# Performance work log

Hardware: AMD Instinct MI355X
Metric: run time of the kernel (lower is better)

## Reference

```python
import jax, jax.numpy as jnp
import numpy as np
import math

N_CELLS = 65536
HIDDEN = 128
IN_DIM = 64
MAX_DEG = 6
BOND_P = 0.5


def _build_graph():
    """2D lattice bond percolation -> padded adjacency [n, MAX_DEG] + signs + mask."""
    rng = np.random.default_rng(0)
    side = int(math.ceil(math.sqrt(N_CELLS)))
    adj = [[] for _ in range(N_CELLS)]
    for i in range(N_CELLS):
        col = i % side
        r = i + 1
        if col + 1 < side and r < N_CELLS and rng.random() < BOND_P:
            adj[i].append(r); adj[r].append(i)
        d = i + side
        if d < N_CELLS and rng.random() < BOND_P:
            adj[i].append(d); adj[d].append(i)
    for i in range(N_CELLS):  # ring fix for isolated nodes
        if not adj[i]:
            r = (i + 1) % N_CELLS
            adj[i].append(r); adj[r].append(i)
    sign_map = {}
    for i in range(N_CELLS):
        for j in adj[i]:
            key = (min(i, j), max(i, j))
            if key not in sign_map:
                sign_map[key] = 1.0 if rng.random() > 0.5 else -1.0
    nbr = np.zeros((N_CELLS, MAX_DEG), np.int32)
    sgn = np.ones((N_CELLS, MAX_DEG), np.float32)
    msk = np.zeros((N_CELLS, MAX_DEG), bool)
    for i in range(N_CELLS):
        for k, j in enumerate(adj[i][:MAX_DEG]):
            nbr[i, k] = j
            msk[i, k] = True
            sgn[i, k] = sign_map[(min(i, j), max(i, j))]
    return nbr, sgn, msk


def setup_inputs() -> dict:
    key = jax.random.key(0)
    ks = jax.random.split(key, 8)
    nbr, sgn, msk = _build_graph()
    n = N_CELLS
    cell_amp = jax.random.uniform(ks[0], (n, HIDDEN)) * 0.5 + 0.5
    cell_phase = jax.random.normal(ks[1], (n, HIDDEN)) * 0.5 \
        + (2.0 * jnp.pi * jnp.arange(n, dtype=jnp.float32) / n)[:, None]
    phase_vel = jax.random.normal(ks[2], (n, HIDDEN)) * 0.05
    return {
        'x': jax.random.normal(ks[3], (1, IN_DIM)),
        'cell_amp': cell_amp.astype(jnp.float32),
        'cell_phase': cell_phase.astype(jnp.float32),
        'phase_vel': phase_vel.astype(jnp.float32),
        'nbr_idx': jnp.asarray(nbr),
        'nbr_sign': jnp.asarray(sgn),
        'nbr_mask': jnp.asarray(msk),
        'W_in': jax.random.normal(ks[4], (HIDDEN, IN_DIM)) * 0.05,
        'b_in': jax.random.normal(ks[5], (HIDDEN,)) * 0.05,
        'W_dec': jax.random.normal(ks[6], (IN_DIM, 2 * HIDDEN)) * 0.05,
        'b_dec': jax.random.normal(ks[7], (IN_DIM,)) * 0.05,
        'step': 1,
    }


def reference(x, cell_amp, cell_phase, phase_vel, nbr_idx, nbr_sign, nbr_mask,
              W_in, b_in, W_dec, b_dec, step):
    n, h = cell_amp.shape
    # complex cell states, then phase-velocity rotation
    states = (cell_amp * jnp.exp(1j * cell_phase)).astype(jnp.complex64)
    states = states * jnp.exp(1j * phase_vel * 0.1)
    ang = jnp.angle(states)                               # [n, h]

    # --- neighbor interference (vectorized gather over padded adjacency) ---
    nbr_states = states[nbr_idx]                          # [n, d, h]
    nbr_ang = ang[nbr_idx]                                # [n, d, h]
    coupling = jnp.cos(ang[:, None, :] - nbr_ang) * nbr_sign[:, :, None]
    contrib = jnp.where(nbr_mask[:, :, None], coupling * nbr_states * 0.1, 0.0)
    interference = contrib.sum(axis=1)                    # [n, h]
    deg = nbr_mask.sum(axis=-1)                           # [n]
    new = 0.7 * states + 0.3 * interference / jnp.maximum(deg, 1)[:, None]
    new = jnp.where((deg > 0)[:, None], new, states)      # 'continue' for isolated nodes

    # --- morphism toward strongest neighbor (argmax over neighbors) ---
    strength = jnp.abs(states).sum(axis=-1)               # [n]
    nstr = jnp.where(nbr_mask, strength[nbr_idx], -jnp.inf)
    best_slot = jnp.argmax(nstr, axis=1)                  # first max, like python max()
    best = jnp.take_along_axis(nbr_idx, best_slot[:, None], axis=1)[:, 0]
    src = states[best]                                    # [n, h]
    morph = jnp.abs(src) * jnp.exp(1j * (jnp.angle(new) - jnp.angle(src)))
    new = jnp.where((deg >= 2)[:, None], new + 0.02 * morph, new)

    # --- global traveling wave ---
    t = step * 0.1
    wave = 0.02 * jnp.sin(t + 2.0 * jnp.pi * jnp.arange(n, dtype=jnp.float32) / n)
    new = new * (1.0 + wave)[:, None]

    # --- input-driven phase perturbation on first 32 cells ---
    sig = x[0] @ W_in.T + b_in                            # [h]
    pp = sig / (jnp.abs(sig).max() + 1e-8) * jnp.pi * 0.1
    idx = jnp.arange(n, dtype=jnp.float32)
    factor = jnp.where(jnp.arange(n) < 32, 0.1 / (1.0 + 0.1 * idx), 0.0)
    new_ang = jnp.angle(new) + pp[None, :] * factor[:, None]
    new = jnp.abs(new) * jnp.exp(1j * new_ang)

    # --- amplitude renormalization per cell ---
    amp = jnp.abs(new)
    amp = amp / (amp.max(axis=-1, keepdims=True) + 1e-8)
    cs = (amp * jnp.exp(1j * jnp.angle(new))).astype(jnp.complex64)

    # --- readout ---
    mean_state = cs.mean(axis=0)                          # [h]
    out_real = jnp.concatenate([mean_state.real, mean_state.imag])[None, :]
    pred = out_real @ W_dec.T + b_dec                     # [1, IN_DIM]
    tension = jnp.var(jnp.abs(cs), ddof=1)                # torch.var (unbiased)
    return pred, tension
```

## Files before the change

kernel.cpp:

```cpp
#include <hip/hip_runtime.h>
#include <hip/hip_fp16.h>
#include <math.h>

#define N_CELLS 65536
#define HIDDEN  128
#define IN_DIM  64
#define MAX_DEG 6

#define WPB    4
#define NPB    32
#define NBLK   (N_CELLS/NPB)
#define CHUNK  4
#define NXCD   8

#define INV2PI 0.15915494309189535f

typedef _Float16 h2f __attribute__((ext_vector_type(2)));
typedef int      i4v __attribute__((ext_vector_type(4)));
typedef float    f4v __attribute__((ext_vector_type(4)));

__device__ __forceinline__ void fsincos(float x, float& s, float& c) {
    const float r = x * INV2PI;
    s = __builtin_amdgcn_sinf(r);
    c = __builtin_amdgcn_cosf(r);
}

#define WS_PP    0
#define WS_FLAG  512
#define WS_STR   1024
#define WS_U     (1024 + N_CELLS*4)
#define WS_V     (WS_U + (size_t)N_CELLS*512)
#define WS_ADJ   (WS_V + (size_t)N_CELLS*512)
#define WS_P     (WS_ADJ + (size_t)N_CELLS*32)
#define WS_SA    (WS_P + 256*NBLK*4)
#define WS_SA2   (WS_SA + NBLK*4)
#define WS_MEAN  (WS_SA2 + NBLK*4)

__global__ __launch_bounds__(256) void k_pre(
    const float* __restrict__ amp, const float* __restrict__ phase,
    const float* __restrict__ vel,
    const float* __restrict__ x, const float* __restrict__ W_in,
    const float* __restrict__ b_in, const unsigned char* __restrict__ maskb,
    int4* __restrict__ U, int4* __restrict__ V, float* __restrict__ strength,
    float* __restrict__ pp, int* __restrict__ flag)
{
    const int tid = threadIdx.x;
    const int bx  = blockIdx.x;
    if (bx < N_CELLS/8) {
        const int blkp = (bx & (NXCD-1)) * (N_CELLS/8/NXCD) + (bx >> 3);
        const int node = blkp*8 + (tid >> 5);
        const int hl   = tid & 31;
        const size_t ro = (size_t)node*HIDDEN + 4*hl;
        const f4v a = __builtin_nontemporal_load((const f4v*)(amp   + ro));
        const f4v p = __builtin_nontemporal_load((const f4v*)(phase + ro));
        const f4v v = __builtin_nontemporal_load((const f4v*)(vel   + ro));
        float s0,c0,s1,c1,s2,c2,s3,c3;
        fsincos(fmaf(0.1f, v.x, p.x), s0, c0);
        fsincos(fmaf(0.1f, v.y, p.y), s1, c1);
        fsincos(fmaf(0.1f, v.z, p.z), s2, c2);
        fsincos(fmaf(0.1f, v.w, p.w), s3, c3);
        union { i4v v4; __half2 h[4]; } uu, vv;
        uu.h[0] = __floats2half2_rn(c0, s0);
        uu.h[1] = __floats2half2_rn(c1, s1);
        uu.h[2] = __floats2half2_rn(c2, s2);
        uu.h[3] = __floats2half2_rn(c3, s3);
        vv.h[0] = __floats2half2_rn(a.x*c0, a.x*s0);
        vv.h[1] = __floats2half2_rn(a.y*c1, a.y*s1);
        vv.h[2] = __floats2half2_rn(a.z*c2, a.z*s2);
        vv.h[3] = __floats2half2_rn(a.w*c3, a.w*s3);
        const size_t base = (size_t)node*32 + hl;
        __builtin_nontemporal_store(uu.v4, (i4v*)(U + base));
        __builtin_nontemporal_store(vv.v4, (i4v*)(V + base));
        float st = a.x + a.y + a.z + a.w;
        #pragma unroll
        for (int off = 16; off > 0; off >>= 1) st += __shfl_xor(st, off);
        if (hl == 0) strength[node] = st;
        return;
    }
    __shared__ float sig[HIDDEN];
    __shared__ float red[HIDDEN];
    __shared__ int fl[256];
    if (tid < HIDDEN) {
        float acc = b_in[tid];
        #pragma unroll 8
        for (int d = 0; d < IN_DIM; ++d) acc = fmaf(W_in[tid*IN_DIM + d], x[d], acc);
        sig[tid] = acc;
        red[tid] = fabsf(acc);
    }
    int v = 0;
    #pragma unroll
    for (int r = 0; r < 4; ++r) v |= (int)maskb[(tid + 256*r)*4 + 1];
    fl[tid] = v;
    __syncthreads();
    for (int s = 64; s > 0; s >>= 1) {
        if (tid < s) red[tid] = fmaxf(red[tid], red[tid + s]);
        __syncthreads();
    }
    for (int s = 128; s > 0; s >>= 1) {
        if (tid < s) fl[tid] |= fl[tid + s];
        __syncthreads();
    }
    if (tid < HIDDEN) pp[tid] = sig[tid] / (red[0] + 1e-8f) * 0.314159265358979f;
    if (tid == 0) *flag = (fl[0] != 0) ? 1 : 0;
}

__global__ __launch_bounds__(256) void k_adj(
    const int* __restrict__ nbr_idx, const float* __restrict__ nbr_sign,
    const void* __restrict__ nbr_mask, const int* __restrict__ flagp,
    const float* __restrict__ strength, int4* __restrict__ adj)
{
    __shared__ int   lw[256][MAX_DEG];
    __shared__ float ls[256][MAX_DEG];
    __shared__ int   ldeg[256];
    const int t = threadIdx.x;
    const int bx = blockIdx.x;
    const int blkp = (bx & (NXCD-1)) * (N_CELLS/256/NXCD) + (bx >> 3);
    const int i = blkp*256 + t;
    const int flagv = *flagp;
    const unsigned char* mb = (const unsigned char*)nbr_mask;
    const int*           mi = (const int*)nbr_mask;
    int cnt = 0;
    #pragma unroll
    for (int k = 0; k < MAX_DEG; ++k) {
        const int e = i*MAX_DEG + k;
        const int m = flagv ? (mb[e] != 0) : (mi[e] != 0);
        const int j = nbr_idx[e];
        const float sg = nbr_sign[e];
        if (m) {
            lw[t][cnt] = j | ((sg < 0.0f) ? (1<<24) : 0) | (1<<25);
            ls[t][cnt] = strength[j];
            ++cnt;
        }
    }
    int cb = 0; float bv = ls[t][0];
    #pragma unroll
    for (int k = 1; k < MAX_DEG; ++k)
        if (k < cnt && ls[t][k] > bv) { bv = ls[t][k]; cb = k; }
    if (cb != 0) {
        const int tmp = lw[t][0];
        lw[t][0] = lw[t][cb];
        lw[t][cb] = tmp;
    }
    #pragma unroll
    for (int k = 0; k < MAX_DEG; ++k) if (k >= cnt) lw[t][k] = i;
    ldeg[t] = cnt;
    __syncthreads();
    const int kmax = max(cnt, ldeg[t ^ 1]);
    adj[2*(size_t)i    ] = make_int4(lw[t][0], lw[t][1], lw[t][2], lw[t][3]);
    adj[2*(size_t)i + 1] = make_int4(lw[t][4], lw[t][5], cnt, kmax);
}

__global__ __launch_bounds__(256) void k_mainc(
    const int4* __restrict__ U, const int4* __restrict__ V,
    const int4* __restrict__ adj,
    const int* __restrict__ step, const float* __restrict__ pp,
    float* __restrict__ P, float* __restrict__ p_sa, float* __restrict__ p_sa2)
{
    __shared__ float4 lredre[WPB][32], lredim[WPB][32];
    __shared__ float  lsa[WPB], lsa2[WPB];

    const int tid   = threadIdx.x;
    const int bx    = blockIdx.x;
    const int blk   = (bx & (NXCD-1)) * (NBLK/NXCD) + (bx >> 3);
    const int node0 = blk * NPB;

    const int wv   = tid >> 6;
    const int lane = tid & 63;
    const int half = lane >> 5;
    const int lh   = lane & 31;
    const float trev = 0.1f * (float)step[0] * INV2PI;
    const float4 ppv = ((const float4*)pp)[lh];

    float accre[4] = {0,0,0,0}, accim[4] = {0,0,0,0};
    float accsa = 0.f, accsa2 = 0.f;

    const int nlbase = wv*(2*CHUNK) + half;
    int4 A0n = adj[2*(size_t)(node0 + nlbase)    ];
    int4 A1n = adj[2*(size_t)(node0 + nlbase) + 1];

    #pragma unroll 1
    for (int c = 0; c < CHUNK; ++c) {
        const int nl = nlbase + 2*c;
        const int i  = node0 + nl;
        const int4 A0 = A0n, A1 = A1n;
        if (c + 1 < CHUNK) {
            A0n = adj[2*(size_t)(i + 2)    ];
            A1n = adj[2*(size_t)(i + 2) + 1];
        }
        const int deg  = A1.z;
        const int kmax = __builtin_amdgcn_readfirstlane(A1.w);
        const int slots[MAX_DEG] = {A0.x, A0.y, A0.z, A0.w, A1.x, A1.y};

        union H { int4 v4; h2f h[4]; };
        H su, sv, nu[MAX_DEG], nv[MAX_DEG];
        const size_t sb = (size_t)(unsigned)i*32 + lh;
        su.v4 = U[sb];
        sv.v4 = V[sb];
        #pragma unroll
        for (int k = 0; k < MAX_DEG; ++k) {
            if (k < kmax) {
                const size_t jb = (size_t)(unsigned)(slots[k] & 0xFFFF)*32 + lh;
                nu[k].v4 = U[jb];
                nv[k].v4 = V[jb];
            }
        }

        h2f acc[4];
        #pragma unroll
        for (int q = 0; q < 4; ++q) acc[q] = (h2f){(_Float16)0.f, (_Float16)0.f};
        #pragma unroll
        for (int k = 0; k < MAX_DEG; ++k) {
            if (k < kmax) {
                const int w = slots[k];
                const float vf = (float)((w >> 25) & 1);
                const float sgnm = (w & (1<<24)) ? -vf : vf;
                #pragma unroll
                for (int q = 0; q < 4; ++q) {
                    const float cosD = __builtin_amdgcn_fdot2(su.h[q], nu[k].h[q], 0.0f, false);
                    const _Float16 t = (_Float16)(cosD * sgnm);
                    const h2f tv = (h2f){t, t};
                    acc[q] = tv * nv[k].h[q] + acc[q];
                }
            }
        }

        const float f = 0.03f * __builtin_amdgcn_rcpf((float)deg);
        float nr[4], ni[4];
        #pragma unroll
        for (int q = 0; q < 4; ++q) {
            nr[q] = fmaf(0.7f, (float)sv.h[q].x, f*(float)acc[q].x);
            ni[q] = fmaf(0.7f, (float)sv.h[q].y, f*(float)acc[q].y);
        }

        const float g2 = (deg >= 2) ? 0.02f : 0.0f;
        #pragma unroll
        for (int q = 0; q < 4; ++q) {
            const float ex = (float)nv[0].h[q].x, ey = (float)nv[0].h[q].y;
            const float im = g2 * __builtin_amdgcn_rsqf(
                fmaxf(nr[q]*nr[q] + ni[q]*ni[q], 1e-30f));
            const float mr = im*(nr[q]*ex + ni[q]*ey);
            const float mi = im*(ni[q]*ex - nr[q]*ey);
            nr[q] += mr; ni[q] += mi;
        }

        const float wr = fmaf((float)i, 1.52587890625e-5f, trev);
        const float wf = 1.0f + 0.02f * __builtin_amdgcn_sinf(wr);
        #pragma unroll
        for (int q = 0; q < 4; ++q) { nr[q] *= wf; ni[q] *= wf; }

        if (i < 32) {
            const float fac = 0.1f / fmaf(0.1f, (float)i, 1.0f);
            const float pv[4] = {ppv.x, ppv.y, ppv.z, ppv.w};
            #pragma unroll
            for (int q = 0; q < 4; ++q) {
                float sp, cp;
                fsincos(pv[q]*fac, sp, cp);
                const float tr = nr[q]*cp - ni[q]*sp;
                ni[q] = ni[q]*cp + nr[q]*sp;
                nr[q] = tr;
            }
        }

        float m[4];
        #pragma unroll
        for (int q = 0; q < 4; ++q) m[q] = sqrtf(nr[q]*nr[q] + ni[q]*ni[q]);
        float lm = fmaxf(fmaxf(m[0], m[1]), fmaxf(m[2], m[3]));
        #pragma unroll
        for (int off = 16; off > 0; off >>= 1) lm = fmaxf(lm, __shfl_xor(lm, off));
        const float sc = 1.0f / (lm + 1e-8f);
        #pragma unroll
        for (int q = 0; q < 4; ++q) {
            accre[q] += nr[q]*sc;
            accim[q] += ni[q]*sc;
            const float A = m[q]*sc;
            accsa  += A;
            accsa2 += A*A;
        }
    }

    #pragma unroll
    for (int q = 0; q < 4; ++q) {
        accre[q] += __shfl_xor(accre[q], 32);
        accim[q] += __shfl_xor(accim[q], 32);
    }
    #pragma unroll
    for (int off = 32; off > 0; off >>= 1) {
        accsa  += __shfl_xor(accsa,  off);
        accsa2 += __shfl_xor(accsa2, off);
    }
    if (half == 0) {
        lredre[wv][lh] = make_float4(accre[0], accre[1], accre[2], accre[3]);
        lredim[wv][lh] = make_float4(accim[0], accim[1], accim[2], accim[3]);
    }
    if (lane == 0) { lsa[wv] = accsa; lsa2[wv] = accsa2; }
    __syncthreads();
    if (tid < 32) {
        float4 r = lredre[0][tid], im = lredim[0][tid];
        #pragma unroll
        for (int w = 1; w < WPB; ++w) {
            const float4 a = lredre[w][tid], b = lredim[w][tid];
            r.x += a.x; r.y += a.y; r.z += a.z; r.w += a.w;
            im.x += b.x; im.y += b.y; im.z += b.z; im.w += b.w;
        }
        P[(4*tid  )*NBLK + blk]       = r.x;
        P[(4*tid+1)*NBLK + blk]       = r.y;
        P[(4*tid+2)*NBLK + blk]       = r.z;
        P[(4*tid+3)*NBLK + blk]       = r.w;
        P[(128+4*tid  )*NBLK + blk]   = im.x;
        P[(128+4*tid+1)*NBLK + blk]   = im.y;
        P[(128+4*tid+2)*NBLK + blk]   = im.z;
        P[(128+4*tid+3)*NBLK + blk]   = im.w;
    }
    if (tid == 0) {
        p_sa [blk] = lsa[0]  + lsa[1]  + lsa[2]  + lsa[3];
        p_sa2[blk] = lsa2[0] + lsa2[1] + lsa2[2] + lsa2[3];
    }
}

__global__ void k_red(const float* __restrict__ P, float* __restrict__ mean)
{
    __shared__ double red[256];
    const int r = blockIdx.x, tid = threadIdx.x;
    double s = 0.0;
    #pragma unroll
    for (int k = 0; k < NBLK/256; ++k) s += (double)P[(size_t)r*NBLK + tid + 256*k];
    red[tid] = s;
    __syncthreads();
    for (int st = 128; st > 0; st >>= 1) { if (tid < st) red[tid] += red[tid + st]; __syncthreads(); }
    if (tid == 0) mean[r] = (float)(red[0] / (double)N_CELLS);
}

__global__ void k_final(const float* __restrict__ mean_in,
                        const float* __restrict__ p_sa, const float* __restrict__ p_sa2,
                        const float* __restrict__ W_dec, const float* __restrict__ b_dec,
                        float* __restrict__ out)
{
    __shared__ float  mean[2*HIDDEN];
    __shared__ double dred[256];
    __shared__ double tots[2];
    const int tid = threadIdx.x;
    mean[tid] = mean_in[tid];
    double sa = 0.0, sa2 = 0.0;
    #pragma unroll
    for (int k = 0; k < NBLK/256; ++k) {
        sa  += (double)p_sa [tid + 256*k];
        sa2 += (double)p_sa2[tid + 256*k];
    }
    dred[tid] = sa;
    __syncthreads();
    for (int s = 128; s > 0; s >>= 1) { if (tid < s) dred[tid] += dred[tid + s]; __syncthreads(); }
    if (tid == 0) tots[0] = dred[0];
    __syncthreads();
    dred[tid] = sa2;
    __syncthreads();
    for (int s = 128; s > 0; s >>= 1) { if (tid < s) dred[tid] += dred[tid + s]; __syncthreads(); }
    if (tid == 0) tots[1] = dred[0];
    __syncthreads();

    if (tid < IN_DIM) {
        float acc = b_dec[tid];
        #pragma unroll 8
        for (int c = 0; c < 2*HIDDEN; ++c) acc = fmaf(mean[c], W_dec[tid*2*HIDDEN + c], acc);
        out[tid] = acc;
    }
    if (tid == 0) {
        const double M = (double)N_CELLS * (double)HIDDEN;
        const double var = (tots[1] - tots[0]*tots[0]/M) / (M - 1.0);
        out[IN_DIM] = (float)var;
    }
}

extern "C" void kernel_launch(void* const* d_in, const int* in_sizes, int n_in,
                              void* d_out, int out_size, void* d_ws, size_t ws_size,
                              hipStream_t stream)
{
    const float* x       = (const float*)d_in[0];
    const float* amp     = (const float*)d_in[1];
    const float* phase   = (const float*)d_in[2];
    const float* vel     = (const float*)d_in[3];
    const int*   nbr_idx = (const int*)d_in[4];
    const float* nbr_sgn = (const float*)d_in[5];
    const void*  nbr_msk = d_in[6];
    const float* W_in    = (const float*)d_in[7];
    const float* b_in    = (const float*)d_in[8];
    const float* W_dec   = (const float*)d_in[9];
    const float* b_dec   = (const float*)d_in[10];
    const int*   step    = (const int*)d_in[11];

    char* wsb = (char*)d_ws;
    float* pp    = (float*)(wsb + WS_PP);
    int*   flag  = (int*)  (wsb + WS_FLAG);
    float* strg  = (float*)(wsb + WS_STR);
    int4*  U     = (int4*) (wsb + WS_U);
    int4*  V     = (int4*) (wsb + WS_V);
    int4*  adjv  = (int4*) (wsb + WS_ADJ);
    float* P     = (float*)(wsb + WS_P);
    float* p_sa  = (float*)(wsb + WS_SA);
    float* p_sa2 = (float*)(wsb + WS_SA2);
    float* meanb = (float*)(wsb + WS_MEAN);
    float* out   = (float*)d_out;

    k_pre<<<N_CELLS/8 + 1, 256, 0, stream>>>(amp, phase, vel, x, W_in, b_in,
                                             (const unsigned char*)nbr_msk,
                                             U, V, strg, pp, flag);
    k_adj<<<N_CELLS/256, 256, 0, stream>>>(nbr_idx, nbr_sgn, nbr_msk, flag, strg, adjv);
    k_mainc<<<NBLK, 256, 0, stream>>>(U, V, adjv, step, pp, P, p_sa, p_sa2);
    k_red<<<256, 256, 0, stream>>>(P, meanb);
    k_final<<<1, 256, 0, stream>>>(meanb, p_sa, p_sa2, W_dec, b_dec, out);
}
```

Measured before the change: 76.20 us.

## Replace complex V buffer with half-precision amplitude array to cut gather bytes

The intermediate V buffer (amp times cos/sin packed as half2, 16 bytes per lane) is replaced by a 4-half amplitude array (8 bytes per lane). The main kernel now rebuilds amplitude-weighted values from U and the amplitude on the fly. This cuts the per-neighbour gather traffic in the main kernel from 32 to 24 bytes per lane and reduces writes in the preprocessing kernel. In exchange it adds a few extra multiplies per neighbour. The nontemporal load and store hints are also dropped in favour of plain accesses.

```diff
diff --git a/kernel.cpp b/kernel.cpp
--- a/kernel.cpp
+++ b/kernel.cpp
@@ -16,8 +16,6 @@
 #define INV2PI 0.15915494309189535f
 
 typedef _Float16 h2f __attribute__((ext_vector_type(2)));
-typedef int      i4v __attribute__((ext_vector_type(4)));
-typedef float    f4v __attribute__((ext_vector_type(4)));
 
 __device__ __forceinline__ void fsincos(float x, float& s, float& c) {
     const float r = x * INV2PI;
@@ -29,8 +27,8 @@
 #define WS_FLAG  512
 #define WS_STR   1024
 #define WS_U     (1024 + N_CELLS*4)
-#define WS_V     (WS_U + (size_t)N_CELLS*512)
-#define WS_ADJ   (WS_V + (size_t)N_CELLS*512)
+#define WS_A     (WS_U + (size_t)N_CELLS*512)
+#define WS_ADJ   (WS_A + (size_t)N_CELLS*256)
 #define WS_P     (WS_ADJ + (size_t)N_CELLS*32)
 #define WS_SA    (WS_P + 256*NBLK*4)
 #define WS_SA2   (WS_SA + NBLK*4)
@@ -41,7 +39,7 @@
     const float* __restrict__ vel,
     const float* __restrict__ x, const float* __restrict__ W_in,
     const float* __restrict__ b_in, const unsigned char* __restrict__ maskb,
-    int4* __restrict__ U, int4* __restrict__ V, float* __restrict__ strength,
+    int4* __restrict__ U, int2* __restrict__ A, float* __restrict__ strength,
     float* __restrict__ pp, int* __restrict__ flag)
 {
     const int tid = threadIdx.x;
@@ -51,26 +49,25 @@
         const int node = blkp*8 + (tid >> 5);
         const int hl   = tid & 31;
         const size_t ro = (size_t)node*HIDDEN + 4*hl;
-        const f4v a = __builtin_nontemporal_load((const f4v*)(amp   + ro));
-        const f4v p = __builtin_nontemporal_load((const f4v*)(phase + ro));
-        const f4v v = __builtin_nontemporal_load((const f4v*)(vel   + ro));
+        const float4 a = *(const float4*)(amp   + ro);
+        const float4 p = *(const float4*)(phase + ro);
+        const float4 v = *(const float4*)(vel   + ro);
         float s0,c0,s1,c1,s2,c2,s3,c3;
         fsincos(fmaf(0.1f, v.x, p.x), s0, c0);
         fsincos(fmaf(0.1f, v.y, p.y), s1, c1);
         fsincos(fmaf(0.1f, v.z, p.z), s2, c2);
         fsincos(fmaf(0.1f, v.w, p.w), s3, c3);
-        union { i4v v4; __half2 h[4]; } uu, vv;
+        union { int4 v4; __half2 h[4]; } uu;
+        union { int2 v2; __half2 h[2]; } aa;
         uu.h[0] = __floats2half2_rn(c0, s0);
         uu.h[1] = __floats2half2_rn(c1, s1);
         uu.h[2] = __floats2half2_rn(c2, s2);
         uu.h[3] = __floats2half2_rn(c3, s3);
-        vv.h[0] = __floats2half2_rn(a.x*c0, a.x*s0);
-        vv.h[1] = __floats2half2_rn(a.y*c1, a.y*s1);
-        vv.h[2] = __floats2half2_rn(a.z*c2, a.z*s2);
-        vv.h[3] = __floats2half2_rn(a.w*c3, a.w*s3);
+        aa.h[0] = __floats2half2_rn(a.x, a.y);
+        aa.h[1] = __floats2half2_rn(a.z, a.w);
         const size_t base = (size_t)node*32 + hl;
-        __builtin_nontemporal_store(uu.v4, (i4v*)(U + base));
-        __builtin_nontemporal_store(vv.v4, (i4v*)(V + base));
+        U[base] = uu.v4;
+        A[base] = aa.v2;
         float st = a.x + a.y + a.z + a.w;
         #pragma unroll
         for (int off = 16; off > 0; off >>= 1) st += __shfl_xor(st, off);
@@ -151,7 +148,7 @@
 }
 
 __global__ __launch_bounds__(256) void k_mainc(
-    const int4* __restrict__ U, const int4* __restrict__ V,
+    const int4* __restrict__ U, const int2* __restrict__ A,
     const int4* __restrict__ adj,
     const int* __restrict__ step, const float* __restrict__ pp,
     float* __restrict__ P, float* __restrict__ p_sa, float* __restrict__ p_sa2)
@@ -191,17 +188,19 @@
         const int kmax = __builtin_amdgcn_readfirstlane(A1.w);
         const int slots[MAX_DEG] = {A0.x, A0.y, A0.z, A0.w, A1.x, A1.y};
 
-        union H { int4 v4; h2f h[4]; };
-        H su, sv, nu[MAX_DEG], nv[MAX_DEG];
+        union HU { int4 v4; h2f h[4]; };
+        union HA { int2 v2; _Float16 a[4]; };
+        HU su, nu[MAX_DEG];
+        HA sa, na[MAX_DEG];
         const size_t sb = (size_t)(unsigned)i*32 + lh;
         su.v4 = U[sb];
-        sv.v4 = V[sb];
+        sa.v2 = A[sb];
         #pragma unroll
         for (int k = 0; k < MAX_DEG; ++k) {
             if (k < kmax) {
                 const size_t jb = (size_t)(unsigned)(slots[k] & 0xFFFF)*32 + lh;
                 nu[k].v4 = U[jb];
-                nv[k].v4 = V[jb];
+                na[k].v2 = A[jb];
             }
         }
 
@@ -217,9 +216,10 @@
                 #pragma unroll
                 for (int q = 0; q < 4; ++q) {
                     const float cosD = __builtin_amdgcn_fdot2(su.h[q], nu[k].h[q], 0.0f, false);
-                    const _Float16 t = (_Float16)(cosD * sgnm);
+                    const float m = cosD * sgnm * (float)na[k].a[q];
+                    const _Float16 t = (_Float16)m;
                     const h2f tv = (h2f){t, t};
-                    acc[q] = tv * nv[k].h[q] + acc[q];
+                    acc[q] = tv * nu[k].h[q] + acc[q];
                 }
             }
         }
@@ -228,14 +228,17 @@
         float nr[4], ni[4];
         #pragma unroll
         for (int q = 0; q < 4; ++q) {
-            nr[q] = fmaf(0.7f, (float)sv.h[q].x, f*(float)acc[q].x);
-            ni[q] = fmaf(0.7f, (float)sv.h[q].y, f*(float)acc[q].y);
+            const float ai = (float)sa.a[q];
+            nr[q] = fmaf(0.7f*ai, (float)su.h[q].x, f*(float)acc[q].x);
+            ni[q] = fmaf(0.7f*ai, (float)su.h[q].y, f*(float)acc[q].y);
         }
 
         const float g2 = (deg >= 2) ? 0.02f : 0.0f;
         #pragma unroll
         for (int q = 0; q < 4; ++q) {
-            const float ex = (float)nv[0].h[q].x, ey = (float)nv[0].h[q].y;
+            const float ab = (float)na[0].a[q];
+            const float ex = ab * (float)nu[0].h[q].x;
+            const float ey = ab * (float)nu[0].h[q].y;
             const float im = g2 * __builtin_amdgcn_rsqf(
                 fmaxf(nr[q]*nr[q] + ni[q]*ni[q], 1e-30f));
             const float mr = im*(nr[q]*ex + ni[q]*ey);
@@ -272,9 +275,9 @@
         for (int q = 0; q < 4; ++q) {
             accre[q] += nr[q]*sc;
             accim[q] += ni[q]*sc;
-            const float A = m[q]*sc;
-            accsa  += A;
-            accsa2 += A*A;
+            const float Av = m[q]*sc;
+            accsa  += Av;
+            accsa2 += Av*Av;
         }
     }
 
@@ -392,7 +395,7 @@
     int*   flag  = (int*)  (wsb + WS_FLAG);
     float* strg  = (float*)(wsb + WS_STR);
     int4*  U     = (int4*) (wsb + WS_U);
-    int4*  V     = (int4*) (wsb + WS_V);
+    int2*  A     = (int2*) (wsb + WS_A);
     int4*  adjv  = (int4*) (wsb + WS_ADJ);
     float* P     = (float*)(wsb + WS_P);
     float* p_sa  = (float*)(wsb + WS_SA);
@@ -402,9 +405,9 @@
 
     k_pre<<<N_CELLS/8 + 1, 256, 0, stream>>>(amp, phase, vel, x, W_in, b_in,
                                              (const unsigned char*)nbr_msk,
-                                             U, V, strg, pp, flag);
+                                             U, A, strg, pp, flag);
     k_adj<<<N_CELLS/256, 256, 0, stream>>>(nbr_idx, nbr_sgn, nbr_msk, flag, strg, adjv);
-    k_mainc<<<NBLK, 256, 0, stream>>>(U, V, adjv, step, pp, P, p_sa, p_sa2);
+    k_mainc<<<NBLK, 256, 0, stream>>>(U, A, adjv, step, pp, P, p_sa, p_sa2);
     k_red<<<256, 256, 0, stream>>>(P, meanb);
     k_final<<<1, 256, 0, stream>>>(meanb, p_sa, p_sa2, W_dec, b_dec, out);
 }
```

Measured after the change: 70.92 us. 6.9% less time.
